# Optimization experiments

Hardware: AMD Instinct MI355X
Metric: run time of the kernel (lower is better)

Reference implementation:

```python
import jax, jax.numpy as jnp
import numpy as np

D_K = 64

def setup_inputs() -> dict:
    key = jax.random.key(0)
    k1, k2, k3, k4 = jax.random.split(key, 4)
    B, H, S = 2, 16, 2048
    Q = jax.random.normal(k1, (B, H, S, D_K), dtype=jnp.float32)
    K = jax.random.normal(k2, (B, H, S, D_K), dtype=jnp.float32)
    V = jax.random.normal(k3, (B, H, S, D_K), dtype=jnp.float32)
    attn_mask = jax.random.randint(k4, (B, H, S, S), 0, 2) == 1
    return {"Q": Q, "K": K, "V": V, "attn_mask": attn_mask}

def reference(Q, K, V, attn_mask):
    scale = 1.0 / np.sqrt(D_K).astype(np.float32)
    # scores: [B, H, S, S]
    scores = jnp.einsum('bhqd,bhkd->bhqk', Q, K) * scale
    scores = jnp.where(attn_mask, jnp.float32(-1e6), scores)
    scores = jax.nn.softmax(scores, axis=-1)
    context = jnp.einsum('bhqk,bhkd->bhqd', scores, V)
    return (context, scores)
```

## Files before the change

kernel.cpp:

```cpp
#include <hip/hip_runtime.h>

#define S_LEN 2048
#define NBH   32

typedef __attribute__((ext_vector_type(8))) __bf16 bf16x8;
typedef __attribute__((ext_vector_type(4))) float  f32x4;

__global__ __launch_bounds__(256) void prep_k(const float* __restrict__ K,
                                              __bf16* __restrict__ kh,
                                              __bf16* __restrict__ kl) {
    const int total = NBH * S_LEN * 64;
    for (int idx = blockIdx.x * 256 + threadIdx.x; idx < total;
         idx += gridDim.x * 256) {
        int d   = idx & 63;
        int key = (idx >> 6) & (S_LEN - 1);
        int bh  = idx >> 17;
        float f = K[idx];
        __bf16 h  = (__bf16)f;
        __bf16 lo = (__bf16)(f - (float)h);
        int dc = d >> 5, g = (d >> 3) & 3, j = d & 7;
        size_t off = ((size_t)((bh * 2 + dc) * S_LEN + key) << 5) + g * 8 + j;
        kh[off] = h;
        kl[off] = lo;
    }
}

__global__ __launch_bounds__(256) void prep_v(const float* __restrict__ V,
                                              __bf16* __restrict__ vb) {
    const int total = NBH * S_LEN * 64;
    for (int idx = blockIdx.x * 256 + threadIdx.x; idx < total;
         idx += gridDim.x * 256) {
        int n  = idx & 63;
        int k  = (idx >> 6) & (S_LEN - 1);
        int bh = idx >> 17;
        float f = V[idx];
        int kc = k >> 5, g = (k >> 3) & 3, j = k & 7;
        size_t off = ((size_t)((bh * 64 + n) * 64 + kc) << 5) + g * 8 + j;
        vb[off] = (__bf16)f;
    }
}

__global__ __launch_bounds__(512) void attn_kernel(
    const float* __restrict__ Q, const int* __restrict__ mask,
    const __bf16* __restrict__ kh, const __bf16* __restrict__ kl,
    const __bf16* __restrict__ vb,
    float* __restrict__ ctxOut, float* __restrict__ scoresOut)
{
    extern __shared__ float lds[];
    __bf16* qf   = (__bf16*)(lds + 32768);
    float*  pmax = lds + 33792;
    float*  psum = lds + 33920;
    float*  mrow = lds + 34048;
    float*  rinv = lds + 34064;
    float*  parts= lds + 34080;

    const int t   = threadIdx.x;
    const int w   = t >> 6;
    const int l   = t & 63;
    const int l15 = l & 15;
    const int lg  = l >> 4;
    const int bh  = blockIdx.y;
    const int q0  = blockIdx.x << 4;

    const int alane = (lg << 4) | ((l15 & 3) << 2) | (l15 >> 2);

    {
        const float* Qg = Q + ((size_t)bh * S_LEN + q0) * 64;
        for (int e = t; e < 16 * 64; e += 512) {
            int row = e >> 6, d = e & 63;
            float fs = Qg[e] * 0.125f;
            __bf16 h  = (__bf16)fs;
            __bf16 lo = (__bf16)(fs - (float)h);
            int dc = d >> 5, g = (d >> 3) & 3, j = d & 7;
            int lane2 = (g << 4) | row;
            qf[((0 + dc) * 64 + lane2) * 8 + j] = h;
            qf[((2 + dc) * 64 + lane2) * 8 + j] = lo;
        }
    }
    __syncthreads();

    {
        bf16x8 ah0 = *(bf16x8*)&qf[(0 * 64 + l) * 8];
        bf16x8 ah1 = *(bf16x8*)&qf[(1 * 64 + l) * 8];
        bf16x8 al0 = *(bf16x8*)&qf[(2 * 64 + l) * 8];
        bf16x8 al1 = *(bf16x8*)&qf[(3 * 64 + l) * 8];

        for (int i = 0; i < 16; ++i) {
            int kt = w + (i << 3);
            int k0 = kt << 4;
            f32x4 acc = {0.f, 0.f, 0.f, 0.f};
            size_t off0 = ((size_t)((bh * 2 + 0) * S_LEN + k0 + l15) << 5) + lg * 8;
            size_t off1 = ((size_t)((bh * 2 + 1) * S_LEN + k0 + l15) << 5) + lg * 8;
            bf16x8 kh0 = *(const bf16x8*)(kh + off0);
            bf16x8 kl0 = *(const bf16x8*)(kl + off0);
            bf16x8 kh1 = *(const bf16x8*)(kh + off1);
            bf16x8 kl1 = *(const bf16x8*)(kl + off1);
            acc = __builtin_amdgcn_mfma_f32_16x16x32_bf16(ah0, kh0, acc, 0, 0, 0);
            acc = __builtin_amdgcn_mfma_f32_16x16x32_bf16(al0, kh0, acc, 0, 0, 0);
            acc = __builtin_amdgcn_mfma_f32_16x16x32_bf16(ah0, kl0, acc, 0, 0, 0);
            acc = __builtin_amdgcn_mfma_f32_16x16x32_bf16(ah1, kh1, acc, 0, 0, 0);
            acc = __builtin_amdgcn_mfma_f32_16x16x32_bf16(al1, kh1, acc, 0, 0, 0);
            acc = __builtin_amdgcn_mfma_f32_16x16x32_bf16(ah1, kl1, acc, 0, 0, 0);

            int col  = k0 + l15;
            int c    = col >> 5;
            int gcol = (col >> 3) & 3;
            int j    = col & 7;
            int base = (c << 9) + (((gcol << 4) | lg) << 3) + j;
            lds[base +  0] = acc[0];
            lds[base + 32] = acc[1];
            lds[base + 64] = acc[2];
            lds[base + 96] = acc[3];
        }
    }
    __syncthreads();

    {
        float mx = -3.0e38f;
        for (int cc = 0; cc < 8; ++cc) {
            int c = (w << 3) + cc;
            int base = (c << 9) + (alane << 3);
            f32x4 v1 = *(f32x4*)&lds[base];
            f32x4 v2 = *(f32x4*)&lds[base + 4];
            mx = fmaxf(mx, fmaxf(fmaxf(v1[0], v1[1]), fmaxf(v1[2], v1[3])));
            mx = fmaxf(mx, fmaxf(fmaxf(v2[0], v2[1]), fmaxf(v2[2], v2[3])));
        }
        mx = fmaxf(mx, __shfl_xor(mx, 16, 64));
        mx = fmaxf(mx, __shfl_xor(mx, 32, 64));
        if (l < 16) pmax[(w << 4) + l] = mx;
    }
    __syncthreads();
    if (t < 16) {
        float m = pmax[t];
        for (int ww = 1; ww < 8; ++ww) m = fmaxf(m, pmax[(ww << 4) + t]);
        mrow[t] = m;
    }
    __syncthreads();

    {
        const int* mbase = mask + (size_t)bh * S_LEN * S_LEN
                                + (size_t)(q0 + l15) * S_LEN;
        float m = mrow[l15];
        float sum = 0.f;
        for (int cc = 0; cc < 8; ++cc) {
            int c = (w << 3) + cc;
            int base = (c << 9) + (alane << 3);
            int colb = (c << 5) + (lg << 3);
            f32x4 v1 = *(f32x4*)&lds[base];
            f32x4 v2 = *(f32x4*)&lds[base + 4];
            int4 m1 = *(const int4*)(mbase + colb);
            int4 m2 = *(const int4*)(mbase + colb + 4);
            f32x4 e1, e2;
            e1[0] = m1.x ? 0.f : __expf(v1[0] - m);
            e1[1] = m1.y ? 0.f : __expf(v1[1] - m);
            e1[2] = m1.z ? 0.f : __expf(v1[2] - m);
            e1[3] = m1.w ? 0.f : __expf(v1[3] - m);
            e2[0] = m2.x ? 0.f : __expf(v2[0] - m);
            e2[1] = m2.y ? 0.f : __expf(v2[1] - m);
            e2[2] = m2.z ? 0.f : __expf(v2[2] - m);
            e2[3] = m2.w ? 0.f : __expf(v2[3] - m);
            *(f32x4*)&lds[base]     = e1;
            *(f32x4*)&lds[base + 4] = e2;
            sum += e1[0] + e1[1] + e1[2] + e1[3]
                 + e2[0] + e2[1] + e2[2] + e2[3];
        }
        sum += __shfl_xor(sum, 16, 64);
        sum += __shfl_xor(sum, 32, 64);
        if (l < 16) psum[(w << 4) + l] = sum;
    }
    __syncthreads();
    if (t < 16) {
        float s = 0.f;
        for (int ww = 0; ww < 8; ++ww) s += psum[(ww << 4) + t];
        rinv[t] = 1.0f / s;
    }
    __syncthreads();

    {
        float rv = rinv[l15];
        float* sbase = scoresOut + (size_t)bh * S_LEN * S_LEN
                                 + (size_t)(q0 + l15) * S_LEN;
        for (int cc = 0; cc < 8; ++cc) {
            int c = (w << 3) + cc;
            int base = (c << 9) + (alane << 3);
            int colb = (c << 5) + (lg << 3);
            f32x4 v1 = *(f32x4*)&lds[base];
            f32x4 v2 = *(f32x4*)&lds[base + 4];
            v1 *= rv;
            v2 *= rv;
            *(f32x4*)(sbase + colb)     = v1;
            *(f32x4*)(sbase + colb + 4) = v2;
        }

        int n0    = (w & 3) << 4;
        int khalf = w >> 2;
        f32x4 acc = {0.f, 0.f, 0.f, 0.f};
        const __bf16* vbase = vb + ((size_t)(bh * 64 + n0 + l15) << 11) + lg * 8;
        for (int cc = 0; cc < 32; ++cc) {
            int c = (khalf << 5) + cc;
            int base = (c << 9) + (alane << 3);
            f32x4 v1 = *(f32x4*)&lds[base];
            f32x4 v2 = *(f32x4*)&lds[base + 4];
            bf16x8 pa;
            pa[0] = (__bf16)v1[0]; pa[1] = (__bf16)v1[1];
            pa[2] = (__bf16)v1[2]; pa[3] = (__bf16)v1[3];
            pa[4] = (__bf16)v2[0]; pa[5] = (__bf16)v2[1];
            pa[6] = (__bf16)v2[2]; pa[7] = (__bf16)v2[3];
            bf16x8 bv = *(const bf16x8*)(vbase + ((size_t)c << 5));
            acc = __builtin_amdgcn_mfma_f32_16x16x32_bf16(pa, bv, acc, 0, 0, 0);
        }
        int pbase = (w << 8) + (lg << 6) + l15;
        parts[pbase +  0] = acc[0];
        parts[pbase + 16] = acc[1];
        parts[pbase + 32] = acc[2];
        parts[pbase + 48] = acc[3];
    }
    __syncthreads();

    {
        float* cbase = ctxOut + ((size_t)bh * S_LEN + q0) * 64;
        for (int e = t; e < 1024; e += 512) {
            int row = e >> 6, d = e & 63;
            int nt = d >> 4, ii = d & 15;
            float v = (parts[(nt << 8) + (row << 4) + ii] +
                       parts[((nt + 4) << 8) + (row << 4) + ii]) * rinv[row];
            cbase[e] = v;
        }
    }
}

extern "C" void kernel_launch(void* const* d_in, const int* in_sizes, int n_in,
                              void* d_out, int out_size, void* d_ws, size_t ws_size,
                              hipStream_t stream) {
    const float* Q    = (const float*)d_in[0];
    const float* K    = (const float*)d_in[1];
    const float* V    = (const float*)d_in[2];
    const int*   mask = (const int*)d_in[3];

    float* ctxOut    = (float*)d_out;
    float* scoresOut = ctxOut + (size_t)NBH * S_LEN * 64;

    __bf16* kh = (__bf16*)d_ws;
    __bf16* kl = kh + (size_t)NBH * S_LEN * 64;
    __bf16* vb = kl + (size_t)NBH * S_LEN * 64;

    prep_k<<<4096, 256, 0, stream>>>(K, kh, kl);
    prep_v<<<4096, 256, 0, stream>>>(V, vb);

    const int lds_bytes = 36128 * 4;
    hipFuncSetAttribute((const void*)attn_kernel,
                        hipFuncAttributeMaxDynamicSharedMemorySize, lds_bytes);

    dim3 grid(S_LEN / 16, NBH);
    attn_kernel<<<grid, 512, lds_bytes, stream>>>(Q, mask, kh, kl, vb,
                                                  ctxOut, scoresOut);
}
```

Measured before the change: 1.380 ms.

## Keep QK scores in registers and stage only bf16 probabilities in LDS

Score tiles from the QK MFMA are now held in registers across max, exp/sum and normalisation, so the fp32 score matrix is no longer staged in LDS. Only bf16 exp values go to LDS, using an XOR swizzle, for the PV MFMA. This roughly halves LDS use to allow more blocks per CU, and launch_bounds(512,4) is added. The cost is higher register pressure (64 accumulator floats per thread), with a risk of spills. Mask reads and score writes become 4-byte per-lane accesses, so they coalesce less than the earlier 16-byte vector accesses.

```diff
diff --git a/kernel.cpp b/kernel.cpp
--- a/kernel.cpp
+++ b/kernel.cpp
@@ -40,19 +40,20 @@
     }
 }
 
-__global__ __launch_bounds__(512) void attn_kernel(
+__global__ __launch_bounds__(512, 4) void attn_kernel(
     const float* __restrict__ Q, const int* __restrict__ mask,
     const __bf16* __restrict__ kh, const __bf16* __restrict__ kl,
     const __bf16* __restrict__ vb,
     float* __restrict__ ctxOut, float* __restrict__ scoresOut)
 {
     extern __shared__ float lds[];
-    __bf16* qf   = (__bf16*)(lds + 32768);
-    float*  pmax = lds + 33792;
-    float*  psum = lds + 33920;
-    float*  mrow = lds + 34048;
-    float*  rinv = lds + 34064;
-    float*  parts= lds + 34080;
+    __bf16* eb   = (__bf16*)lds;
+    __bf16* qf   = (__bf16*)(lds + 16384);
+    float*  pmax = lds + 17408;
+    float*  psum = lds + 17536;
+    float*  mrow = lds + 17664;
+    float*  rinv = lds + 17680;
+    float*  parts= lds + 17696;
 
     const int t   = threadIdx.x;
     const int w   = t >> 6;
@@ -62,10 +63,9 @@
     const int bh  = blockIdx.y;
     const int q0  = blockIdx.x << 4;
 
-    const int alane = (lg << 4) | ((l15 & 3) << 2) | (l15 >> 2);
-
     {
         const float* Qg = Q + ((size_t)bh * S_LEN + q0) * 64;
+        #pragma unroll
         for (int e = t; e < 16 * 64; e += 512) {
             int row = e >> 6, d = e & 63;
             float fs = Qg[e] * 0.125f;
@@ -79,55 +79,52 @@
     }
     __syncthreads();
 
+    f32x4 acc[16];
     {
         bf16x8 ah0 = *(bf16x8*)&qf[(0 * 64 + l) * 8];
         bf16x8 ah1 = *(bf16x8*)&qf[(1 * 64 + l) * 8];
         bf16x8 al0 = *(bf16x8*)&qf[(2 * 64 + l) * 8];
         bf16x8 al1 = *(bf16x8*)&qf[(3 * 64 + l) * 8];
 
+        #pragma unroll
         for (int i = 0; i < 16; ++i) {
             int kt = w + (i << 3);
             int k0 = kt << 4;
-            f32x4 acc = {0.f, 0.f, 0.f, 0.f};
+            f32x4 a = {0.f, 0.f, 0.f, 0.f};
             size_t off0 = ((size_t)((bh * 2 + 0) * S_LEN + k0 + l15) << 5) + lg * 8;
             size_t off1 = ((size_t)((bh * 2 + 1) * S_LEN + k0 + l15) << 5) + lg * 8;
             bf16x8 kh0 = *(const bf16x8*)(kh + off0);
             bf16x8 kl0 = *(const bf16x8*)(kl + off0);
             bf16x8 kh1 = *(const bf16x8*)(kh + off1);
             bf16x8 kl1 = *(const bf16x8*)(kl + off1);
-            acc = __builtin_amdgcn_mfma_f32_16x16x32_bf16(ah0, kh0, acc, 0, 0, 0);
-            acc = __builtin_amdgcn_mfma_f32_16x16x32_bf16(al0, kh0, acc, 0, 0, 0);
-            acc = __builtin_amdgcn_mfma_f32_16x16x32_bf16(ah0, kl0, acc, 0, 0, 0);
-            acc = __builtin_amdgcn_mfma_f32_16x16x32_bf16(ah1, kh1, acc, 0, 0, 0);
-            acc = __builtin_amdgcn_mfma_f32_16x16x32_bf16(al1, kh1, acc, 0, 0, 0);
-            acc = __builtin_amdgcn_mfma_f32_16x16x32_bf16(ah1, kl1, acc, 0, 0, 0);
-
-            int col  = k0 + l15;
-            int c    = col >> 5;
-            int gcol = (col >> 3) & 3;
-            int j    = col & 7;
-            int base = (c << 9) + (((gcol << 4) | lg) << 3) + j;
-            lds[base +  0] = acc[0];
-            lds[base + 32] = acc[1];
-            lds[base + 64] = acc[2];
-            lds[base + 96] = acc[3];
-        }
-    }
-    __syncthreads();
-
-    {
-        float mx = -3.0e38f;
-        for (int cc = 0; cc < 8; ++cc) {
-            int c = (w << 3) + cc;
-            int base = (c << 9) + (alane << 3);
-            f32x4 v1 = *(f32x4*)&lds[base];
-            f32x4 v2 = *(f32x4*)&lds[base + 4];
-            mx = fmaxf(mx, fmaxf(fmaxf(v1[0], v1[1]), fmaxf(v1[2], v1[3])));
-            mx = fmaxf(mx, fmaxf(fmaxf(v2[0], v2[1]), fmaxf(v2[2], v2[3])));
-        }
-        mx = fmaxf(mx, __shfl_xor(mx, 16, 64));
-        mx = fmaxf(mx, __shfl_xor(mx, 32, 64));
-        if (l < 16) pmax[(w << 4) + l] = mx;
+            a = __builtin_amdgcn_mfma_f32_16x16x32_bf16(ah0, kh0, a, 0, 0, 0);
+            a = __builtin_amdgcn_mfma_f32_16x16x32_bf16(al0, kh0, a, 0, 0, 0);
+            a = __builtin_amdgcn_mfma_f32_16x16x32_bf16(ah0, kl0, a, 0, 0, 0);
+            a = __builtin_amdgcn_mfma_f32_16x16x32_bf16(ah1, kh1, a, 0, 0, 0);
+            a = __builtin_amdgcn_mfma_f32_16x16x32_bf16(al1, kh1, a, 0, 0, 0);
+            a = __builtin_amdgcn_mfma_f32_16x16x32_bf16(ah1, kl1, a, 0, 0, 0);
+            acc[i] = a;
+        }
+    }
+
+    {
+        f32x4 mx = acc[0];
+        #pragma unroll
+        for (int i = 1; i < 16; ++i) {
+            mx[0] = fmaxf(mx[0], acc[i][0]);
+            mx[1] = fmaxf(mx[1], acc[i][1]);
+            mx[2] = fmaxf(mx[2], acc[i][2]);
+            mx[3] = fmaxf(mx[3], acc[i][3]);
+        }
+        #pragma unroll
+        for (int r = 0; r < 4; ++r) {
+            float v = mx[r];
+            v = fmaxf(v, __shfl_xor(v, 1, 64));
+            v = fmaxf(v, __shfl_xor(v, 2, 64));
+            v = fmaxf(v, __shfl_xor(v, 4, 64));
+            v = fmaxf(v, __shfl_xor(v, 8, 64));
+            if (l15 == 0) pmax[(w << 4) + (lg << 2) + r] = v;
+        }
     }
     __syncthreads();
     if (t < 16) {
@@ -138,35 +135,43 @@
     __syncthreads();
 
     {
-        const int* mbase = mask + (size_t)bh * S_LEN * S_LEN
-                                + (size_t)(q0 + l15) * S_LEN;
-        float m = mrow[l15];
-        float sum = 0.f;
-        for (int cc = 0; cc < 8; ++cc) {
-            int c = (w << 3) + cc;
-            int base = (c << 9) + (alane << 3);
-            int colb = (c << 5) + (lg << 3);
-            f32x4 v1 = *(f32x4*)&lds[base];
-            f32x4 v2 = *(f32x4*)&lds[base + 4];
-            int4 m1 = *(const int4*)(mbase + colb);
-            int4 m2 = *(const int4*)(mbase + colb + 4);
-            f32x4 e1, e2;
-            e1[0] = m1.x ? 0.f : __expf(v1[0] - m);
-            e1[1] = m1.y ? 0.f : __expf(v1[1] - m);
-            e1[2] = m1.z ? 0.f : __expf(v1[2] - m);
-            e1[3] = m1.w ? 0.f : __expf(v1[3] - m);
-            e2[0] = m2.x ? 0.f : __expf(v2[0] - m);
-            e2[1] = m2.y ? 0.f : __expf(v2[1] - m);
-            e2[2] = m2.z ? 0.f : __expf(v2[2] - m);
-            e2[3] = m2.w ? 0.f : __expf(v2[3] - m);
-            *(f32x4*)&lds[base]     = e1;
-            *(f32x4*)&lds[base + 4] = e2;
-            sum += e1[0] + e1[1] + e1[2] + e1[3]
-                 + e2[0] + e2[1] + e2[2] + e2[3];
-        }
-        sum += __shfl_xor(sum, 16, 64);
-        sum += __shfl_xor(sum, 32, 64);
-        if (l < 16) psum[(w << 4) + l] = sum;
+        float mr0 = mrow[(lg << 2) + 0];
+        float mr1 = mrow[(lg << 2) + 1];
+        float mr2 = mrow[(lg << 2) + 2];
+        float mr3 = mrow[(lg << 2) + 3];
+        const int* mb = mask + (size_t)bh * S_LEN * S_LEN
+                             + (size_t)(q0 + (lg << 2)) * S_LEN + l15;
+        f32x4 sum = {0.f, 0.f, 0.f, 0.f};
+        #pragma unroll
+        for (int i = 0; i < 16; ++i) {
+            int kt = w + (i << 3);
+            int k0 = kt << 4;
+            int gc = ((kt & 1) << 1) | (l15 >> 3);
+            int ebase = ((kt >> 1) << 9) | (gc << 7) | ((lg ^ gc) << 3) | (l15 & 7);
+            int m0 = mb[(size_t)0 * S_LEN + k0];
+            int m1 = mb[(size_t)1 * S_LEN + k0];
+            int m2 = mb[(size_t)2 * S_LEN + k0];
+            int m3 = mb[(size_t)3 * S_LEN + k0];
+            float e0 = m0 ? 0.f : __expf(acc[i][0] - mr0);
+            float e1 = m1 ? 0.f : __expf(acc[i][1] - mr1);
+            float e2 = m2 ? 0.f : __expf(acc[i][2] - mr2);
+            float e3 = m3 ? 0.f : __expf(acc[i][3] - mr3);
+            acc[i][0] = e0; acc[i][1] = e1; acc[i][2] = e2; acc[i][3] = e3;
+            sum[0] += e0; sum[1] += e1; sum[2] += e2; sum[3] += e3;
+            eb[ebase +  0] = (__bf16)e0;
+            eb[ebase + 32] = (__bf16)e1;
+            eb[ebase + 64] = (__bf16)e2;
+            eb[ebase + 96] = (__bf16)e3;
+        }
+        #pragma unroll
+        for (int r = 0; r < 4; ++r) {
+            float v = sum[r];
+            v += __shfl_xor(v, 1, 64);
+            v += __shfl_xor(v, 2, 64);
+            v += __shfl_xor(v, 4, 64);
+            v += __shfl_xor(v, 8, 64);
+            if (l15 == 0) psum[(w << 4) + (lg << 2) + r] = v;
+        }
     }
     __syncthreads();
     if (t < 16) {
@@ -177,48 +182,47 @@
     __syncthreads();
 
     {
-        float rv = rinv[l15];
-        float* sbase = scoresOut + (size_t)bh * S_LEN * S_LEN
-                                 + (size_t)(q0 + l15) * S_LEN;
-        for (int cc = 0; cc < 8; ++cc) {
-            int c = (w << 3) + cc;
-            int base = (c << 9) + (alane << 3);
-            int colb = (c << 5) + (lg << 3);
-            f32x4 v1 = *(f32x4*)&lds[base];
-            f32x4 v2 = *(f32x4*)&lds[base + 4];
-            v1 *= rv;
-            v2 *= rv;
-            *(f32x4*)(sbase + colb)     = v1;
-            *(f32x4*)(sbase + colb + 4) = v2;
-        }
-
+        float rv0 = rinv[(lg << 2) + 0];
+        float rv1 = rinv[(lg << 2) + 1];
+        float rv2 = rinv[(lg << 2) + 2];
+        float rv3 = rinv[(lg << 2) + 3];
+        float* sb = scoresOut + (size_t)bh * S_LEN * S_LEN
+                              + (size_t)(q0 + (lg << 2)) * S_LEN + l15;
+        #pragma unroll
+        for (int i = 0; i < 16; ++i) {
+            int k0 = (w + (i << 3)) << 4;
+            sb[(size_t)0 * S_LEN + k0] = acc[i][0] * rv0;
+            sb[(size_t)1 * S_LEN + k0] = acc[i][1] * rv1;
+            sb[(size_t)2 * S_LEN + k0] = acc[i][2] * rv2;
+            sb[(size_t)3 * S_LEN + k0] = acc[i][3] * rv3;
+        }
+    }
+
+    {
         int n0    = (w & 3) << 4;
         int khalf = w >> 2;
-        f32x4 acc = {0.f, 0.f, 0.f, 0.f};
+        const int alane  = (lg << 4) | ((l15 & 3) << 2) | (l15 >> 2);
+        const int alane2 = alane ^ lg;
+        f32x4 o = {0.f, 0.f, 0.f, 0.f};
         const __bf16* vbase = vb + ((size_t)(bh * 64 + n0 + l15) << 11) + lg * 8;
+        #pragma unroll
         for (int cc = 0; cc < 32; ++cc) {
             int c = (khalf << 5) + cc;
-            int base = (c << 9) + (alane << 3);
-            f32x4 v1 = *(f32x4*)&lds[base];
-            f32x4 v2 = *(f32x4*)&lds[base + 4];
-            bf16x8 pa;
-            pa[0] = (__bf16)v1[0]; pa[1] = (__bf16)v1[1];
-            pa[2] = (__bf16)v1[2]; pa[3] = (__bf16)v1[3];
-            pa[4] = (__bf16)v2[0]; pa[5] = (__bf16)v2[1];
-            pa[6] = (__bf16)v2[2]; pa[7] = (__bf16)v2[3];
+            bf16x8 pa = *(bf16x8*)&eb[(c << 9) + (alane2 << 3)];
             bf16x8 bv = *(const bf16x8*)(vbase + ((size_t)c << 5));
-            acc = __builtin_amdgcn_mfma_f32_16x16x32_bf16(pa, bv, acc, 0, 0, 0);
+            o = __builtin_amdgcn_mfma_f32_16x16x32_bf16(pa, bv, o, 0, 0, 0);
         }
         int pbase = (w << 8) + (lg << 6) + l15;
-        parts[pbase +  0] = acc[0];
-        parts[pbase + 16] = acc[1];
-        parts[pbase + 32] = acc[2];
-        parts[pbase + 48] = acc[3];
+        parts[pbase +  0] = o[0];
+        parts[pbase + 16] = o[1];
+        parts[pbase + 32] = o[2];
+        parts[pbase + 48] = o[3];
     }
     __syncthreads();
 
     {
         float* cbase = ctxOut + ((size_t)bh * S_LEN + q0) * 64;
+        #pragma unroll
         for (int e = t; e < 1024; e += 512) {
             int row = e >> 6, d = e & 63;
             int nt = d >> 4, ii = d & 15;
@@ -247,7 +251,7 @@
     prep_k<<<4096, 256, 0, stream>>>(K, kh, kl);
     prep_v<<<4096, 256, 0, stream>>>(V, vb);
 
-    const int lds_bytes = 36128 * 4;
+    const int lds_bytes = 19744 * 4;
     hipFuncSetAttribute((const void*)attn_kernel,
                         hipFuncAttributeMaxDynamicSharedMemorySize, lds_bytes);
 
```

Result: faster. 1.170 ms (-15.2%).
